# Optimization experiments

Hardware: AMD Instinct MI355X
Metric: run time of the kernel (lower is better)

## Reference

```python
import jax, jax.numpy as jnp
import numpy as np
from jax import lax

B, N, CIN, MID, OUT, G, H, CHILDS = 16, 1024, 256, 512, 256, 4, 1, 512


def _ln(x, g, b, eps=1e-6):
    m = x.mean(-1, keepdims=True)
    v = ((x - m) ** 2).mean(-1, keepdims=True)
    return (x - m) / jnp.sqrt(v + eps) * g + b


def _gconv(x, W, b):
    # grouped 1x1 conv1d: x [B,Cin,N], W [Cout, Cin//G], b [Cout]
    Bb, Cin, Nn = x.shape
    Cout = W.shape[0]
    xg = x.reshape(Bb, G, Cin // G, Nn)
    Wg = W.reshape(G, Cout // G, Cin // G)
    y = jnp.einsum('bgcn,goc->bgon', xg, Wg).reshape(Bb, Cout, Nn)
    return y + b[None, :, None]


def _forward(x, masks_roi1, masks_roi2, score_mask, gt_feat,
             W_att, b_att, W1, b1, W2, b2, g1, beta1, g2, beta2, Wg, bg):
    dt = x.dtype
    # gt branch
    gts = jax.nn.relu(gt_feat @ Wg + bg)  # [B,N,OUT]

    mr1 = masks_roi1 * score_mask[:, None, :]
    mr2 = masks_roi2 * score_mask[:, None, :]

    # attention logits without materializing the [B,N,N,2C] concat:
    # ft[b,i,j] = cat(x[b,j], x[b,i]);  logits = ft @ W_att + b_att
    Wq, Wk = W_att[:CIN], W_att[CIN:]
    lj = jnp.einsum('bjc,ch->bjh', x, Wq)  # query part (varies over j)
    li = jnp.einsum('bic,ch->bih', x, Wk)  # key part   (varies over i)
    attn = jax.nn.sigmoid(lj[:, None, :, :] + li[:, :, None, :] + b_att)  # [B,N,N,H]

    attn1 = attn * mr1[:, :, :, None]
    attn2 = attn * mr2[:, :, :, None]

    # torch fancy-index assign atten_mask[:,:,idces,:]=1 reduces to: any column
    # index appearing in ANY topk index set gets 1 along dim 2 for all b,i,h.
    k4, k2 = CHILDS // 4, CHILDS // 2
    a1 = jnp.moveaxis(attn1, 2, 3)  # [B,N,H,N] -> topk over last axis (= dim 2)
    a2 = jnp.moveaxis(attn2, 2, 3)
    idx1 = lax.top_k(a1, k4)[1]
    idx1m = lax.top_k(-a1, k4)[1]
    idx2 = lax.top_k(a2, k2)[1]
    idx2m = lax.top_k(-a2, k4)[1]
    all_idx = jnp.concatenate([idx1.ravel(), idx1m.ravel(), idx2.ravel(), idx2m.ravel()])
    col = jnp.zeros((N,), dtype=dt).at[all_idx].set(1.0)

    attn = attn * (mr1 + mr2)[:, :, :, None] * col[None, None, :, None]

    f = (score_mask == 0).astype(dt)  # [B,N]
    f_diag = f[:, :, None] * jnp.eye(N, dtype=dt)  # diag_embed
    atten = (attn + f_diag[:, :, :, None]) / CHILDS
    atten = jnp.transpose(atten, (0, 3, 2, 1))  # [B,H,Nj,Ni]

    x_t = jnp.transpose(x, (0, 2, 1))  # [B,CIN,N]
    o1 = jax.nn.relu(_gconv(x_t, W1, b1))  # [B,MID,N]
    o1m = jnp.matmul(o1.reshape(B, H, MID // H, N), atten).reshape(B, MID, N)
    o1m = _ln(jnp.transpose(o1m, (0, 2, 1)), g1, beta1)  # [B,N,MID]
    o1 = o1 + jnp.transpose(o1m, (0, 2, 1))

    o2 = jax.nn.relu(_gconv(o1, W2, b2))  # [B,OUT,N]
    o2m = jnp.matmul(o2.reshape(B, H, OUT // H, N), atten).reshape(B, OUT, N)
    node_feat = _ln(jnp.transpose(o2m, (0, 2, 1)), g2, beta2)  # [B,N,OUT]
    o2 = o2 + jnp.transpose(node_feat, (0, 2, 1))
    output2 = jnp.transpose(o2, (0, 2, 1))  # [B,N,OUT]
    return output2, gts, node_feat


def setup_inputs() -> dict:
    key = jax.random.key(0)
    ks = jax.random.split(key, 16)
    x = jax.random.normal(ks[0], (B, N, CIN), jnp.float32)
    masks_roi1 = (jax.random.uniform(ks[1], (B, N, N)) < 0.1).astype(jnp.float32)
    masks_roi2 = (jax.random.uniform(ks[2], (B, N, N)) < 0.1).astype(jnp.float32)
    score_mask = (jax.random.uniform(ks[3], (B, N)) < 0.8).astype(jnp.float32)
    gt_feat = jax.random.normal(ks[4], (B, N, CIN), jnp.float32)
    s = 0.05
    W_att = jax.random.normal(ks[5], (2 * CIN, H), jnp.float32) * s
    b_att = jnp.zeros((H,), jnp.float32)
    W1 = jax.random.normal(ks[6], (MID, CIN // G), jnp.float32) * s
    b1 = jax.random.normal(ks[7], (MID,), jnp.float32) * s
    W2 = jax.random.normal(ks[8], (OUT, MID // G), jnp.float32) * s
    b2 = jax.random.normal(ks[9], (OUT,), jnp.float32) * s
    g1 = jax.random.normal(ks[10], (MID,), jnp.float32) * s
    beta1 = jnp.zeros((MID,), jnp.float32)
    g2 = jax.random.normal(ks[11], (OUT,), jnp.float32) * s
    beta2 = jnp.zeros((OUT,), jnp.float32)
    Wg = jax.random.normal(ks[12], (CIN, OUT), jnp.float32) * s
    bg = jax.random.normal(ks[13], (OUT,), jnp.float32) * s
    return {"x": x, "masks_roi1": masks_roi1, "masks_roi2": masks_roi2,
            "score_mask": score_mask, "gt_feat": gt_feat,
            "W_att": W_att, "b_att": b_att, "W1": W1, "b1": b1,
            "W2": W2, "b2": b2, "g1": g1, "beta1": beta1,
            "g2": g2, "beta2": beta2, "Wg": Wg, "bg": bg}


def reference(x, masks_roi1, masks_roi2, score_mask, gt_feat,
              W_att, b_att, W1, b1, W2, b2, g1, beta1, g2, beta2, Wg, bg):
    return _forward(x, masks_roi1, masks_roi2, score_mask, gt_feat,
                    W_att, b_att, W1, b1, W2, b2, g1, beta1, g2, beta2, Wg, bg)
```

## Files before the change

kernel.cpp:

```cpp
#include <hip/hip_runtime.h>
#include <cstddef>
#include <cstdint>

#define B_ 16
#define N_ 1024
#define CIN_ 256
#define MID_ 512
#define OUT_ 256

typedef __attribute__((ext_vector_type(8))) short short8v;
typedef __attribute__((ext_vector_type(4))) float f32x4;

__device__ __forceinline__ float sigf(float z){ return 1.f/(1.f+expf(-z)); }
__device__ __forceinline__ ushort f2bf(float f){
  uint32_t u=__float_as_uint(f);
  uint32_t r=(u + 0x7fffu + ((u>>16)&1u))>>16;
  return (ushort)r;
}
__device__ __forceinline__ float bf2f(ushort u){ return __uint_as_float(((uint32_t)u)<<16); }

__device__ __forceinline__ void async16(void* lds, const void* g){
  __builtin_amdgcn_global_load_lds(
      (const __attribute__((address_space(1))) uint32_t*)g,
      (__attribute__((address_space(3))) uint32_t*)lds,
      16, 0, 0);
}

__global__ __launch_bounds__(256) void k_prep(const float* __restrict__ x,
    const float* __restrict__ Watt, float* __restrict__ lj, float* __restrict__ li)
{
  int bn = blockIdx.x*256 + threadIdx.x;
  const float4* xr = (const float4*)(x + (size_t)bn*CIN_);
  const float4* wq = (const float4*)(Watt);
  const float4* wk = (const float4*)(Watt + CIN_);
  float aq=0.f, ak=0.f;
  #pragma unroll 8
  for(int c=0;c<CIN_/4;++c){
    float4 xv=xr[c]; float4 q=wq[c]; float4 w=wk[c];
    aq += xv.x*q.x+xv.y*q.y+xv.z*q.z+xv.w*q.w;
    ak += xv.x*w.x+xv.y*w.y+xv.z*w.z+xv.w*w.w;
  }
  lj[bn]=aq; li[bn]=ak;
}

__global__ __launch_bounds__(256) void k_cast2(const float* __restrict__ x,
    const float* __restrict__ gt, ushort* __restrict__ xb, ushort* __restrict__ gtb)
{
  int i = blockIdx.x*256 + threadIdx.x;
  int which = i>>20; int idx = i & 1048575;
  float4 v = ((const float4*)(which ? gt : x))[idx];
  ((ushort4*)(which ? gtb : xb))[idx] = make_ushort4(f2bf(v.x), f2bf(v.y), f2bf(v.z), f2bf(v.w));
}

__global__ __launch_bounds__(256) void k_wcast(const float* __restrict__ W1,
    const float* __restrict__ W2, const float* __restrict__ Wg,
    ushort* __restrict__ W1b, ushort* __restrict__ W2b, ushort* __restrict__ WgTb)
{
  int bid=blockIdx.x, t=threadIdx.x;
  if(bid<128){ int i=bid*256+t; W1b[i]=f2bf(W1[i]); }
  else if(bid<256){ int i=(bid-128)*256+t; W2b[i]=f2bf(W2[i]); }
  else { int idx=(bid-256)*256+t; int o=idx>>8, c=idx&255; WgTb[idx]=f2bf(Wg[(size_t)c*OUT_+o]); }
}

__global__ __launch_bounds__(256) void k_col(
    const float* __restrict__ m1, const float* __restrict__ m2,
    const float* __restrict__ sc, const float* __restrict__ lj,
    const float* __restrict__ li, const float* __restrict__ batt,
    float* __restrict__ colf, ushort* __restrict__ mrs)
{
  int wid = threadIdx.x>>6, lane = threadIdx.x&63;
  int row = blockIdx.x*4 + wid; int b = row>>10;
  size_t base = (size_t)row*N_ + lane*16;
  const float4* m1p = (const float4*)(m1+base);
  const float4* m2p = (const float4*)(m2+base);
  const float4* scp = (const float4*)(sc + (b<<10) + lane*16);
  float mr1[16], mr2[16];
  int z1=0, z2=0;
  #pragma unroll
  for(int q=0;q<4;++q){
    float4 a=m1p[q], c=m2p[q], s=scp[q];
    mr1[4*q+0]=a.x*s.x; mr1[4*q+1]=a.y*s.y; mr1[4*q+2]=a.z*s.z; mr1[4*q+3]=a.w*s.w;
    mr2[4*q+0]=c.x*s.x; mr2[4*q+1]=c.y*s.y; mr2[4*q+2]=c.z*s.z; mr2[4*q+3]=c.w*s.w;
    #pragma unroll
    for(int k=0;k<4;++k){ z1 += (mr1[4*q+k]==0.f); z2 += (mr2[4*q+k]==0.f); }
  }
  ushort mb[16];
  #pragma unroll
  for(int k=0;k<16;++k) mb[k]=f2bf(mr1[k]+mr2[k]);
  *(short8v*)(mrs+base)   = *(short8v*)&mb[0];
  *(short8v*)(mrs+base+8) = *(short8v*)&mb[8];
  int s1=z1, s2=z2;
  #pragma unroll
  for(int off=1; off<64; off<<=1){
    int t1=__shfl_up(s1,off), t2=__shfl_up(s2,off);
    if(lane>=off){ s1+=t1; s2+=t2; }
  }
  int excl1=s1-z1, excl2=s2-z2;
  int Z1=__shfl(s1,63), Z2=__shfl(s2,63);
  int P1=1024-Z1, P2=1024-Z2;
  bool rare = (P1>128)||(P2>256)||(Z1<128)||(Z2<128);
  if(!rare){
    int zb1=excl1, zb2=excl2;
    #pragma unroll
    for(int k=0;k<16;++k){
      bool q = (mr1[k]!=0.f) || (zb1<128) || (mr2[k]!=0.f) || (zb2<128) || (P2+zb2<256);
      if(q) colf[lane*16+k]=1.0f;
      zb1 += (mr1[k]==0.f); zb2 += (mr2[k]==0.f);
    }
  } else {
    float lir=li[row], ba=batt[0];
    const float* m1r = m1 + (size_t)row*N_;
    const float* m2r = m2 + (size_t)row*N_;
    const float* scr = sc + (b<<10);
    const float* ljr = lj + (b<<10);
    float a1v[16], a2v[16];
    #pragma unroll
    for(int k=0;k<16;++k){
      float v = sigf(ljr[lane*16+k]+lir+ba);
      a1v[k]=mr1[k]*v; a2v[k]=mr2[k]*v;
    }
    for(int k=0;k<16;++k){
      int j = lane*16+k;
      int c1=0,c1m=0,c2=0,c2m=0;
      for(int jp=0;jp<N_;++jp){
        float sv=scr[jp];
        float vv=sigf(ljr[jp]+lir+ba);
        float p1=m1r[jp]*sv*vv, p2=m2r[jp]*sv*vv;
        bool lo = jp<j;
        c1 += (p1>a1v[k])||((p1==a1v[k])&&lo);
        c1m+= (p1<a1v[k])||((p1==a1v[k])&&lo);
        c2 += (p2>a2v[k])||((p2==a2v[k])&&lo);
        c2m+= (p2<a2v[k])||((p2==a2v[k])&&lo);
      }
      if(c1<128||c1m<128||c2<256||c2m<128) colf[j]=1.0f;
    }
  }
}

__global__ __launch_bounds__(256) void k_at(const ushort* __restrict__ mrs,
    const float* __restrict__ sc, const float* __restrict__ lj,
    const float* __restrict__ li, const float* __restrict__ batt,
    const float* __restrict__ colf, ushort* __restrict__ Atb)
{
  int row=blockIdx.x, t=threadIdx.x; int b=row>>10, i=row&1023;
  size_t base=(size_t)row*N_ + 4*t;
  ushort4 mv=*(const ushort4*)(mrs+base);
  float4 ljv=*(const float4*)(lj + (b<<10) + 4*t);
  float4 cv =*(const float4*)(colf + 4*t);
  float lir=li[row], ba=batt[0];
  float fi = (sc[(b<<10)+i]==0.f)?1.f:0.f;
  float mra[4]={bf2f(mv.x),bf2f(mv.y),bf2f(mv.z),bf2f(mv.w)};
  float ljr[4]={ljv.x,ljv.y,ljv.z,ljv.w};
  float cr[4]={cv.x,cv.y,cv.z,cv.w};
  ushort o[4]; int j0=4*t;
  #pragma unroll
  for(int k=0;k<4;++k){
    float v=sigf(ljr[k]+lir+ba);
    float val=v*mra[k]*cr[k];
    if(j0+k==i) val+=fi;
    o[k]=f2bf(val*(1.f/512.f));
  }
  *(ushort4*)(Atb+base) = make_ushort4(o[0],o[1],o[2],o[3]);
}

template<int BM,int BN,int WR,int WC>
__global__ __launch_bounds__(256) void mgemm(
    const ushort* __restrict__ A, int lda, long long sAb, long long sAg,
    const ushort* __restrict__ Bp, int ldb, long long sBb, long long sBg,
    float* __restrict__ C, ushort* __restrict__ Cb, int ldc, long long sCb, long long sCg,
    int K, int nG,
    const float* __restrict__ biasM, int biasMG,
    const float* __restrict__ biasN, int relu)
{
  static_assert(WR*WC==4 && BM==WR*64 && BN==WC*64, "tile");
  __shared__ __align__(16) ushort As[BM*32];
  __shared__ __align__(16) ushort Bs[BN*32];
  int z=blockIdx.z, b=z/nG, g=z%nG;
  A  += (size_t)b*sAb + (size_t)g*sAg;
  Bp += (size_t)b*sBb + (size_t)g*sBg;
  size_t cOff = (size_t)b*sCb + (size_t)g*sCg;
  int m0 = blockIdx.y*BM, n0 = blockIdx.x*BN;
  int tid=threadIdx.x, w=tid>>6, lane=tid&63;
  int la=lane&15, hi=lane>>4;
  int wr=w/WC, wc=w%WC;
  f32x4 acc[4][4] = {};
  constexpr int RND = (BM+BN)/64;
  int srow = lane>>2;
  int sk8  = (lane&3)*8;
  for(int k0=0;k0<K;k0+=32){
    #pragma unroll
    for(int r=0;r<RND;++r){
      int row0 = r*64 + w*16;
      if(row0 < BM){
        const ushort* src = A + (size_t)(m0+row0+srow)*lda + k0 + sk8;
        async16((char*)As + row0*64, src);
      } else {
        const ushort* src = Bp + (size_t)(n0+row0-BM+srow)*ldb + k0 + sk8;
        async16((char*)Bs + (row0-BM)*64, src);
      }
    }
    __syncthreads();
    short8v af[4], bf4[4];
    #pragma unroll
    for(int i2=0;i2<4;++i2) af[i2] = *(const short8v*)&As[(wr*64+i2*16+la)*32 + hi*8];
    #pragma unroll
    for(int j2=0;j2<4;++j2) bf4[j2] = *(const short8v*)&Bs[(wc*64+j2*16+la)*32 + hi*8];
    #pragma unroll
    for(int i2=0;i2<4;++i2)
      #pragma unroll
      for(int j2=0;j2<4;++j2)
        acc[i2][j2] = __builtin_amdgcn_mfma_f32_16x16x32_bf16(af[i2], bf4[j2], acc[i2][j2], 0,0,0);
    __syncthreads();
  }
  #pragma unroll
  for(int i2=0;i2<4;++i2){
    int row0 = m0 + wr*64 + i2*16 + hi*4;
    #pragma unroll
    for(int j2=0;j2<4;++j2){
      int col = n0 + wc*64 + j2*16 + la;
      float bn = biasN ? biasN[col] : 0.f;
      #pragma unroll
      for(int r=0;r<4;++r){
        int row = row0 + r;
        float v = acc[i2][j2][r] + bn + (biasM ? biasM[(size_t)g*biasMG + row] : 0.f);
        if(relu) v = fmaxf(v, 0.f);
        if(C)  C [cOff + (size_t)row*ldc + col] = v;
        if(Cb) Cb[cOff + (size_t)row*ldc + col] = f2bf(v);
      }
    }
  }
}

__global__ __launch_bounds__(256) void k_ln1(const float* __restrict__ o1mT,
    const ushort* __restrict__ o1b,
    const float* __restrict__ g1v, const float* __restrict__ be1, ushort* __restrict__ o1pb)
{
  int row=blockIdx.x, t=threadIdx.x; int b=row>>10, i=row&1023;
  float2 v = ((const float2*)(o1mT + (size_t)row*MID_))[t];
  float s=v.x+v.y, s2=v.x*v.x+v.y*v.y;
  for(int off=32; off; off>>=1){ s+=__shfl_down(s,off); s2+=__shfl_down(s2,off); }
  __shared__ float sm[8];
  int lane=t&63, wid=t>>6;
  if(lane==0){ sm[wid]=s; sm[4+wid]=s2; }
  __syncthreads();
  s=sm[0]+sm[1]+sm[2]+sm[3]; s2=sm[4]+sm[5]+sm[6]+sm[7];
  float mean=s*(1.f/MID_), var=s2*(1.f/MID_)-mean*mean;
  float rstd=rsqrtf(var+1e-6f);
  int m0=2*t;
  float a0=(v.x-mean)*rstd*g1v[m0]+be1[m0];
  float a1=(v.y-mean)*rstd*g1v[m0+1]+be1[m0+1];
  float r0 = bf2f(o1b[((size_t)(b*MID_+m0  ))*N_ + i]);
  float r1 = bf2f(o1b[((size_t)(b*MID_+m0+1))*N_ + i]);
  ushort2 o; o.x=f2bf(a0+r0); o.y=f2bf(a1+r1);
  ((ushort2*)(o1pb + (size_t)row*MID_))[t] = o;
}

__global__ __launch_bounds__(256) void k_ln2f(const float* __restrict__ o2mT,
    const ushort* __restrict__ o2b,
    const float* __restrict__ g2v, const float* __restrict__ be2,
    float* __restrict__ node, float* __restrict__ out2)
{
  int row=blockIdx.x, t=threadIdx.x; int b=row>>10, i=row&1023;
  float v = o2mT[(size_t)row*OUT_ + t];
  float s=v, s2=v*v;
  for(int off=32; off; off>>=1){ s+=__shfl_down(s,off); s2+=__shfl_down(s2,off); }
  __shared__ float sm[8];
  int lane=t&63, wid=t>>6;
  if(lane==0){ sm[wid]=s; sm[4+wid]=s2; }
  __syncthreads();
  s=sm[0]+sm[1]+sm[2]+sm[3]; s2=sm[4]+sm[5]+sm[6]+sm[7];
  float mean=s*(1.f/OUT_); float var=s2*(1.f/OUT_)-mean*mean;
  float rstd=rsqrtf(var+1e-6f);
  float nf=(v-mean)*rstd*g2v[t]+be2[t];
  size_t ro=(size_t)row*OUT_+t;
  node[ro]=nf;
  out2[ro]=nf + bf2f(o2b[((size_t)(b*OUT_+t))*N_ + i]);
}

extern "C" void kernel_launch(void* const* d_in, const int* in_sizes, int n_in,
                              void* d_out, int out_size, void* d_ws, size_t ws_size,
                              hipStream_t stream)
{
  const float* x    = (const float*)d_in[0];
  const float* m1   = (const float*)d_in[1];
  const float* m2   = (const float*)d_in[2];
  const float* sc   = (const float*)d_in[3];
  const float* gt   = (const float*)d_in[4];
  const float* Watt = (const float*)d_in[5];
  const float* batt = (const float*)d_in[6];
  const float* W1   = (const float*)d_in[7];
  const float* b1   = (const float*)d_in[8];
  const float* W2   = (const float*)d_in[9];
  const float* b2   = (const float*)d_in[10];
  const float* g1   = (const float*)d_in[11];
  const float* be1  = (const float*)d_in[12];
  const float* g2   = (const float*)d_in[13];
  const float* be2  = (const float*)d_in[14];
  const float* Wg   = (const float*)d_in[15];
  const float* bg   = (const float*)d_in[16];

  float* out2 = (float*)d_out;
  float* gtso = out2 + (size_t)B_*N_*OUT_;
  float* node = gtso + (size_t)B_*N_*OUT_;

  char* ws = (char*)d_ws;
  float*  colf = (float*)(ws);
  float*  lj   = (float*)(ws + 4096);
  float*  li   = (float*)(ws + 69632);
  ushort* W1b  = (ushort*)(ws + 135168);
  ushort* W2b  = (ushort*)(ws + 200704);
  ushort* WgTb = (ushort*)(ws + 266240);
  char* R1 = ws + 1048576;
  ushort* mrs  = (ushort*)R1;
  float*  o1mT = (float*)R1;
  ushort* Atb  = (ushort*)(ws + 34603008);
  char* R3 = ws + 68157440;
  ushort* xb  = (ushort*)R3;
  ushort* gtb = (ushort*)(R3 + 8388608);
  ushort* o2b = (ushort*)R3;
  ushort* o1b = (ushort*)(ws + 84934656);
  char* R5 = ws + 101711872;
  ushort* o1pb = (ushort*)R5;
  float*  o2mT = (float*)R5;

  hipMemsetAsync(colf, 0, 4096, stream);
  k_prep <<<dim3(B_*N_/256),dim3(256),0,stream>>>(x,Watt,lj,li);
  k_cast2<<<dim3(8192),dim3(256),0,stream>>>(x, gt, xb, gtb);
  k_wcast<<<dim3(512),dim3(256),0,stream>>>(W1, W2, Wg, W1b, W2b, WgTb);
  k_col  <<<dim3(B_*N_/4),dim3(256),0,stream>>>(m1,m2,sc,lj,li,batt,colf,mrs);
  k_at   <<<dim3(B_*N_),dim3(256),0,stream>>>(mrs,sc,lj,li,batt,colf,Atb);

  mgemm<128,128,2,2><<<dim3(2,128,1),256,0,stream>>>(
      gtb, CIN_, 0,0,
      WgTb, CIN_, 0,0,
      gtso, (ushort*)0, OUT_, 0,0,
      CIN_, 1, nullptr,0, bg, 1);

  mgemm<128,128,2,2><<<dim3(8,1,B_*4),256,0,stream>>>(
      W1b, 64, 0, (long long)128*64,
      xb, CIN_, (long long)N_*CIN_, 64,
      (float*)0, o1b, N_, (long long)MID_*N_, (long long)128*N_,
      64, 4, b1, 128, nullptr, 1);

  mgemm<128,128,2,2><<<dim3(4,8,B_),256,0,stream>>>(
      Atb, N_, (long long)N_*N_, 0,
      o1b, N_, (long long)MID_*N_, 0,
      o1mT, (ushort*)0, MID_, (long long)N_*MID_, 0,
      N_, 1, nullptr,0, nullptr, 0);

  k_ln1<<<dim3(B_*N_),256,0,stream>>>(o1mT, o1b, g1, be1, o1pb);

  mgemm<64,256,1,4><<<dim3(4,1,B_*4),256,0,stream>>>(
      W2b, 128, 0, (long long)64*128,
      o1pb, MID_, (long long)N_*MID_, 128,
      (float*)0, o2b, N_, (long long)OUT_*N_, (long long)64*N_,
      128, 4, b2, 64, nullptr, 1);

  mgemm<128,128,2,2><<<dim3(2,8,B_),256,0,stream>>>(
      Atb, N_, (long long)N_*N_, 0,
      o2b, N_, (long long)OUT_*N_, 0,
      o2mT, (ushort*)0, OUT_, (long long)N_*OUT_, 0,
      N_, 1, nullptr,0, nullptr, 0);

  k_ln2f<<<dim3(B_*N_),256,0,stream>>>(o2mT, o2b, g2, be2, node, out2);
}
```

Measured before the change: 465.2 us.

## Fuse prep/cast kernels, widen GEMM K-tile, emit transposed residuals, rework column mask

The separate projection and cast kernels are merged into one kernel that uses a wave per row with a shuffle reduction. The column-mask kernel now assigns one block per row, with a cross-wave prefix scan and a single fused pass over j'. The GEMM takes a K-tile of 64 and a flat async-load mapping, so each stage does more MFMA work per barrier. The o1/o2 GEMMs also write a transposed bf16 copy so the layer-norm kernels can read residuals coalesced instead of with strided gathers. The cost is extra epilogue writes, with uncoalesced transposed stores, plus more LDS per block.

Result: faster. 398.4 us (-14.4%).

```diff
diff --git a/kernel.cpp b/kernel.cpp
--- a/kernel.cpp
+++ b/kernel.cpp
@@ -26,30 +26,30 @@
       16, 0, 0);
 }
 
-__global__ __launch_bounds__(256) void k_prep(const float* __restrict__ x,
-    const float* __restrict__ Watt, float* __restrict__ lj, float* __restrict__ li)
-{
-  int bn = blockIdx.x*256 + threadIdx.x;
-  const float4* xr = (const float4*)(x + (size_t)bn*CIN_);
-  const float4* wq = (const float4*)(Watt);
-  const float4* wk = (const float4*)(Watt + CIN_);
-  float aq=0.f, ak=0.f;
-  #pragma unroll 8
-  for(int c=0;c<CIN_/4;++c){
-    float4 xv=xr[c]; float4 q=wq[c]; float4 w=wk[c];
-    aq += xv.x*q.x+xv.y*q.y+xv.z*q.z+xv.w*q.w;
-    ak += xv.x*w.x+xv.y*w.y+xv.z*w.z+xv.w*w.w;
-  }
-  lj[bn]=aq; li[bn]=ak;
-}
-
-__global__ __launch_bounds__(256) void k_cast2(const float* __restrict__ x,
-    const float* __restrict__ gt, ushort* __restrict__ xb, ushort* __restrict__ gtb)
-{
-  int i = blockIdx.x*256 + threadIdx.x;
-  int which = i>>20; int idx = i & 1048575;
-  float4 v = ((const float4*)(which ? gt : x))[idx];
-  ((ushort4*)(which ? gtb : xb))[idx] = make_ushort4(f2bf(v.x), f2bf(v.y), f2bf(v.z), f2bf(v.w));
+__global__ __launch_bounds__(256) void k_pc(const float* __restrict__ x,
+    const float* __restrict__ gt, const float* __restrict__ Watt,
+    float* __restrict__ lj, float* __restrict__ li,
+    ushort* __restrict__ xb, ushort* __restrict__ gtb)
+{
+  int bid=blockIdx.x, wid=threadIdx.x>>6, lane=threadIdx.x&63;
+  if(bid < 4096){
+    int row = bid*4 + wid;
+    float4 xv = ((const float4*)(x + (size_t)row*CIN_))[lane];
+    ((ushort4*)(xb + (size_t)row*CIN_))[lane] =
+        make_ushort4(f2bf(xv.x), f2bf(xv.y), f2bf(xv.z), f2bf(xv.w));
+    float4 q = ((const float4*)Watt)[lane];
+    float4 w = ((const float4*)(Watt + CIN_))[lane];
+    float aq = xv.x*q.x+xv.y*q.y+xv.z*q.z+xv.w*q.w;
+    float ak = xv.x*w.x+xv.y*w.y+xv.z*w.z+xv.w*w.w;
+    #pragma unroll
+    for(int off=32; off; off>>=1){ aq += __shfl_xor(aq,off); ak += __shfl_xor(ak,off); }
+    if(lane==0){ lj[row]=aq; li[row]=ak; }
+  } else {
+    int row = (bid-4096)*4 + wid;
+    float4 v = ((const float4*)(gt + (size_t)row*CIN_))[lane];
+    ((ushort4*)(gtb + (size_t)row*CIN_))[lane] =
+        make_ushort4(f2bf(v.x), f2bf(v.y), f2bf(v.z), f2bf(v.w));
+  }
 }
 
 __global__ __launch_bounds__(256) void k_wcast(const float* __restrict__ W1,
@@ -68,43 +68,43 @@
     const float* __restrict__ li, const float* __restrict__ batt,
     float* __restrict__ colf, ushort* __restrict__ mrs)
 {
-  int wid = threadIdx.x>>6, lane = threadIdx.x&63;
-  int row = blockIdx.x*4 + wid; int b = row>>10;
-  size_t base = (size_t)row*N_ + lane*16;
-  const float4* m1p = (const float4*)(m1+base);
-  const float4* m2p = (const float4*)(m2+base);
-  const float4* scp = (const float4*)(sc + (b<<10) + lane*16);
-  float mr1[16], mr2[16];
-  int z1=0, z2=0;
-  #pragma unroll
-  for(int q=0;q<4;++q){
-    float4 a=m1p[q], c=m2p[q], s=scp[q];
-    mr1[4*q+0]=a.x*s.x; mr1[4*q+1]=a.y*s.y; mr1[4*q+2]=a.z*s.z; mr1[4*q+3]=a.w*s.w;
-    mr2[4*q+0]=c.x*s.x; mr2[4*q+1]=c.y*s.y; mr2[4*q+2]=c.z*s.z; mr2[4*q+3]=c.w*s.w;
-    #pragma unroll
-    for(int k=0;k<4;++k){ z1 += (mr1[4*q+k]==0.f); z2 += (mr2[4*q+k]==0.f); }
-  }
-  ushort mb[16];
-  #pragma unroll
-  for(int k=0;k<16;++k) mb[k]=f2bf(mr1[k]+mr2[k]);
-  *(short8v*)(mrs+base)   = *(short8v*)&mb[0];
-  *(short8v*)(mrs+base+8) = *(short8v*)&mb[8];
-  int s1=z1, s2=z2;
+  int row = blockIdx.x; int b = row >> 10; int t = threadIdx.x;
+  int lane = t&63, wid = t>>6;
+  size_t base = (size_t)row*N_ + 4*t;
+  float4 m1v = *(const float4*)(m1 + base);
+  float4 m2v = *(const float4*)(m2 + base);
+  float4 scv = *(const float4*)(sc + (b<<10) + 4*t);
+  float mr1[4] = {m1v.x*scv.x, m1v.y*scv.y, m1v.z*scv.z, m1v.w*scv.w};
+  float mr2[4] = {m2v.x*scv.x, m2v.y*scv.y, m2v.z*scv.z, m2v.w*scv.w};
+  *(ushort4*)(mrs + base) = make_ushort4(f2bf(mr1[0]+mr2[0]), f2bf(mr1[1]+mr2[1]),
+                                         f2bf(mr1[2]+mr2[2]), f2bf(mr1[3]+mr2[3]));
+  int z1=0,z2=0;
+  #pragma unroll
+  for(int k=0;k<4;++k){ z1 += (mr1[k]==0.f); z2 += (mr2[k]==0.f); }
+  int s = z1 | (z2<<16);
   #pragma unroll
   for(int off=1; off<64; off<<=1){
-    int t1=__shfl_up(s1,off), t2=__shfl_up(s2,off);
-    if(lane>=off){ s1+=t1; s2+=t2; }
-  }
-  int excl1=s1-z1, excl2=s2-z2;
-  int Z1=__shfl(s1,63), Z2=__shfl(s2,63);
-  int P1=1024-Z1, P2=1024-Z2;
+    int u = __shfl_up(s,off);
+    if(lane>=off) s += u;
+  }
+  __shared__ int wsum[4];
+  if(lane==63) wsum[wid]=s;
+  __syncthreads();
+  int prev=0, tot=0;
+  #pragma unroll
+  for(int w2=0;w2<4;++w2){ int v=wsum[w2]; tot+=v; if(w2<wid) prev+=v; }
+  int incl = s + prev;
+  int z1i = incl & 0xffff, z2i = incl >> 16;
+  int excl1 = z1i - z1, excl2 = z2i - z2;
+  int Z1 = tot & 0xffff, Z2 = tot >> 16;
+  int P1 = 1024-Z1, P2 = 1024-Z2;
   bool rare = (P1>128)||(P2>256)||(Z1<128)||(Z2<128);
   if(!rare){
     int zb1=excl1, zb2=excl2;
     #pragma unroll
-    for(int k=0;k<16;++k){
+    for(int k=0;k<4;++k){
       bool q = (mr1[k]!=0.f) || (zb1<128) || (mr2[k]!=0.f) || (zb2<128) || (P2+zb2<256);
-      if(q) colf[lane*16+k]=1.0f;
+      if(q) colf[4*t+k]=1.0f;
       zb1 += (mr1[k]==0.f); zb2 += (mr2[k]==0.f);
     }
   } else {
@@ -113,27 +113,28 @@
     const float* m2r = m2 + (size_t)row*N_;
     const float* scr = sc + (b<<10);
     const float* ljr = lj + (b<<10);
-    float a1v[16], a2v[16];
-    #pragma unroll
-    for(int k=0;k<16;++k){
-      float v = sigf(ljr[lane*16+k]+lir+ba);
+    float a1v[4], a2v[4];
+    #pragma unroll
+    for(int k=0;k<4;++k){
+      float v = sigf(ljr[4*t+k]+lir+ba);
       a1v[k]=mr1[k]*v; a2v[k]=mr2[k]*v;
     }
-    for(int k=0;k<16;++k){
-      int j = lane*16+k;
-      int c1=0,c1m=0,c2=0,c2m=0;
-      for(int jp=0;jp<N_;++jp){
-        float sv=scr[jp];
-        float vv=sigf(ljr[jp]+lir+ba);
-        float p1=m1r[jp]*sv*vv, p2=m2r[jp]*sv*vv;
-        bool lo = jp<j;
-        c1 += (p1>a1v[k])||((p1==a1v[k])&&lo);
-        c1m+= (p1<a1v[k])||((p1==a1v[k])&&lo);
-        c2 += (p2>a2v[k])||((p2==a2v[k])&&lo);
-        c2m+= (p2<a2v[k])||((p2==a2v[k])&&lo);
+    int c1[4]={0,0,0,0}, c1m[4]={0,0,0,0}, c2[4]={0,0,0,0}, c2m[4]={0,0,0,0};
+    for(int jp=0;jp<N_;++jp){
+      float vv = sigf(ljr[jp]+lir+ba);
+      float p1 = m1r[jp]*scr[jp]*vv, p2 = m2r[jp]*scr[jp]*vv;
+      #pragma unroll
+      for(int k=0;k<4;++k){
+        bool lo = jp < 4*t+k;
+        c1[k] += (p1>a1v[k])||((p1==a1v[k])&&lo);
+        c1m[k]+= (p1<a1v[k])||((p1==a1v[k])&&lo);
+        c2[k] += (p2>a2v[k])||((p2==a2v[k])&&lo);
+        c2m[k]+= (p2<a2v[k])||((p2==a2v[k])&&lo);
       }
-      if(c1<128||c1m<128||c2<256||c2m<128) colf[j]=1.0f;
-    }
+    }
+    #pragma unroll
+    for(int k=0;k<4;++k)
+      if(c1[k]<128||c1m[k]<128||c2[k]<256||c2m[k]<128) colf[4*t+k]=1.0f;
   }
 }
 
@@ -163,53 +164,57 @@
   *(ushort4*)(Atb+base) = make_ushort4(o[0],o[1],o[2],o[3]);
 }
 
-template<int BM,int BN,int WR,int WC>
+template<int BM,int BN,int WR,int WC,int BK>
 __global__ __launch_bounds__(256) void mgemm(
     const ushort* __restrict__ A, int lda, long long sAb, long long sAg,
     const ushort* __restrict__ Bp, int ldb, long long sBb, long long sBg,
     float* __restrict__ C, ushort* __restrict__ Cb, int ldc, long long sCb, long long sCg,
+    ushort* __restrict__ CbT, long long sTb, long long sTg, int ldt,
     int K, int nG,
     const float* __restrict__ biasM, int biasMG,
     const float* __restrict__ biasN, int relu)
 {
   static_assert(WR*WC==4 && BM==WR*64 && BN==WC*64, "tile");
-  __shared__ __align__(16) ushort As[BM*32];
-  __shared__ __align__(16) ushort Bs[BN*32];
+  static_assert((BM*BK)%512==0 && (BN*BK)%512==0, "stage align");
+  __shared__ __align__(16) ushort As[BM*BK];
+  __shared__ __align__(16) ushort Bs[BN*BK];
   int z=blockIdx.z, b=z/nG, g=z%nG;
   A  += (size_t)b*sAb + (size_t)g*sAg;
   Bp += (size_t)b*sBb + (size_t)g*sBg;
   size_t cOff = (size_t)b*sCb + (size_t)g*sCg;
+  size_t tOff = (size_t)b*sTb + (size_t)g*sTg;
   int m0 = blockIdx.y*BM, n0 = blockIdx.x*BN;
   int tid=threadIdx.x, w=tid>>6, lane=tid&63;
   int la=lane&15, hi=lane>>4;
   int wr=w/WC, wc=w%WC;
   f32x4 acc[4][4] = {};
-  constexpr int RND = (BM+BN)/64;
-  int srow = lane>>2;
-  int sk8  = (lane&3)*8;
-  for(int k0=0;k0<K;k0+=32){
-    #pragma unroll
-    for(int r=0;r<RND;++r){
-      int row0 = r*64 + w*16;
-      if(row0 < BM){
-        const ushort* src = A + (size_t)(m0+row0+srow)*lda + k0 + sk8;
-        async16((char*)As + row0*64, src);
+  constexpr int ISS = (BM+BN)*BK/2048;
+  for(int k0=0;k0<K;k0+=BK){
+    #pragma unroll
+    for(int r=0;r<ISS;++r){
+      int e = (r*256 + tid)*8;
+      if(e < BM*BK){
+        int row=e/BK, kk=e%BK;
+        async16((char*)As + (size_t)e*2, A + (size_t)(m0+row)*lda + k0+kk);
       } else {
-        const ushort* src = Bp + (size_t)(n0+row0-BM+srow)*ldb + k0 + sk8;
-        async16((char*)Bs + (row0-BM)*64, src);
+        int e2=e-BM*BK; int row=e2/BK, kk=e2%BK;
+        async16((char*)Bs + (size_t)e2*2, Bp + (size_t)(n0+row)*ldb + k0+kk);
       }
     }
     __syncthreads();
-    short8v af[4], bf4[4];
-    #pragma unroll
-    for(int i2=0;i2<4;++i2) af[i2] = *(const short8v*)&As[(wr*64+i2*16+la)*32 + hi*8];
-    #pragma unroll
-    for(int j2=0;j2<4;++j2) bf4[j2] = *(const short8v*)&Bs[(wc*64+j2*16+la)*32 + hi*8];
-    #pragma unroll
-    for(int i2=0;i2<4;++i2)
-      #pragma unroll
-      for(int j2=0;j2<4;++j2)
-        acc[i2][j2] = __builtin_amdgcn_mfma_f32_16x16x32_bf16(af[i2], bf4[j2], acc[i2][j2], 0,0,0);
+    #pragma unroll
+    for(int h=0;h<BK/32;++h){
+      short8v af[4], bf4[4];
+      #pragma unroll
+      for(int i2=0;i2<4;++i2) af[i2] = *(const short8v*)&As[(wr*64+i2*16+la)*BK + h*32 + hi*8];
+      #pragma unroll
+      for(int j2=0;j2<4;++j2) bf4[j2] = *(const short8v*)&Bs[(wc*64+j2*16+la)*BK + h*32 + hi*8];
+      #pragma unroll
+      for(int i2=0;i2<4;++i2)
+        #pragma unroll
+        for(int j2=0;j2<4;++j2)
+          acc[i2][j2] = __builtin_amdgcn_mfma_f32_16x16x32_bf16(af[i2], bf4[j2], acc[i2][j2], 0,0,0);
+    }
     __syncthreads();
   }
   #pragma unroll
@@ -224,18 +229,19 @@
         int row = row0 + r;
         float v = acc[i2][j2][r] + bn + (biasM ? biasM[(size_t)g*biasMG + row] : 0.f);
         if(relu) v = fmaxf(v, 0.f);
-        if(C)  C [cOff + (size_t)row*ldc + col] = v;
-        if(Cb) Cb[cOff + (size_t)row*ldc + col] = f2bf(v);
+        if(C)   C  [cOff + (size_t)row*ldc + col] = v;
+        if(Cb)  Cb [cOff + (size_t)row*ldc + col] = f2bf(v);
+        if(CbT) CbT[tOff + (size_t)col*ldt + row] = f2bf(v);
       }
     }
   }
 }
 
 __global__ __launch_bounds__(256) void k_ln1(const float* __restrict__ o1mT,
-    const ushort* __restrict__ o1b,
+    const ushort* __restrict__ o1bT,
     const float* __restrict__ g1v, const float* __restrict__ be1, ushort* __restrict__ o1pb)
 {
-  int row=blockIdx.x, t=threadIdx.x; int b=row>>10, i=row&1023;
+  int row=blockIdx.x, t=threadIdx.x;
   float2 v = ((const float2*)(o1mT + (size_t)row*MID_))[t];
   float s=v.x+v.y, s2=v.x*v.x+v.y*v.y;
   for(int off=32; off; off>>=1){ s+=__shfl_down(s,off); s2+=__shfl_down(s2,off); }
@@ -249,18 +255,17 @@
   int m0=2*t;
   float a0=(v.x-mean)*rstd*g1v[m0]+be1[m0];
   float a1=(v.y-mean)*rstd*g1v[m0+1]+be1[m0+1];
-  float r0 = bf2f(o1b[((size_t)(b*MID_+m0  ))*N_ + i]);
-  float r1 = bf2f(o1b[((size_t)(b*MID_+m0+1))*N_ + i]);
-  ushort2 o; o.x=f2bf(a0+r0); o.y=f2bf(a1+r1);
+  ushort2 rr = ((const ushort2*)(o1bT + (size_t)row*MID_))[t];
+  ushort2 o; o.x=f2bf(a0+bf2f(rr.x)); o.y=f2bf(a1+bf2f(rr.y));
   ((ushort2*)(o1pb + (size_t)row*MID_))[t] = o;
 }
 
 __global__ __launch_bounds__(256) void k_ln2f(const float* __restrict__ o2mT,
-    const ushort* __restrict__ o2b,
+    const ushort* __restrict__ o2bT,
     const float* __restrict__ g2v, const float* __restrict__ be2,
     float* __restrict__ node, float* __restrict__ out2)
 {
-  int row=blockIdx.x, t=threadIdx.x; int b=row>>10, i=row&1023;
+  int row=blockIdx.x, t=threadIdx.x;
   float v = o2mT[(size_t)row*OUT_ + t];
   float s=v, s2=v*v;
   for(int off=32; off; off>>=1){ s+=__shfl_down(s,off); s2+=__shfl_down(s2,off); }
@@ -274,7 +279,7 @@
   float nf=(v-mean)*rstd*g2v[t]+be2[t];
   size_t ro=(size_t)row*OUT_+t;
   node[ro]=nf;
-  out2[ro]=nf + bf2f(o2b[((size_t)(b*OUT_+t))*N_ + i]);
+  out2[ro]=nf + bf2f(o2bT[ro]);
 }
 
 extern "C" void kernel_launch(void* const* d_in, const int* in_sizes, int n_in,
@@ -315,52 +320,59 @@
   float*  o1mT = (float*)R1;
   ushort* Atb  = (ushort*)(ws + 34603008);
   char* R3 = ws + 68157440;
-  ushort* xb  = (ushort*)R3;
-  ushort* gtb = (ushort*)(R3 + 8388608);
-  ushort* o2b = (ushort*)R3;
-  ushort* o1b = (ushort*)(ws + 84934656);
+  ushort* xb   = (ushort*)R3;
+  ushort* gtb  = (ushort*)(R3 + 8388608);
+  ushort* o2b  = (ushort*)R3;
+  ushort* o2bT = (ushort*)(R3 + 8388608);
+  char* R4 = ws + 84934656;
+  ushort* o1b  = (ushort*)R4;
+  ushort* o1pb = (ushort*)R4;
   char* R5 = ws + 101711872;
-  ushort* o1pb = (ushort*)R5;
+  ushort* o1bT = (ushort*)R5;
   float*  o2mT = (float*)R5;
 
   hipMemsetAsync(colf, 0, 4096, stream);
-  k_prep <<<dim3(B_*N_/256),dim3(256),0,stream>>>(x,Watt,lj,li);
-  k_cast2<<<dim3(8192),dim3(256),0,stream>>>(x, gt, xb, gtb);
+  k_pc   <<<dim3(8192),dim3(256),0,stream>>>(x, gt, Watt, lj, li, xb, gtb);
   k_wcast<<<dim3(512),dim3(256),0,stream>>>(W1, W2, Wg, W1b, W2b, WgTb);
-  k_col  <<<dim3(B_*N_/4),dim3(256),0,stream>>>(m1,m2,sc,lj,li,batt,colf,mrs);
+  k_col  <<<dim3(B_*N_),dim3(256),0,stream>>>(m1,m2,sc,lj,li,batt,colf,mrs);
   k_at   <<<dim3(B_*N_),dim3(256),0,stream>>>(mrs,sc,lj,li,batt,colf,Atb);
 
-  mgemm<128,128,2,2><<<dim3(2,128,1),256,0,stream>>>(
+  mgemm<128,128,2,2,64><<<dim3(2,128,1),256,0,stream>>>(
       gtb, CIN_, 0,0,
       WgTb, CIN_, 0,0,
       gtso, (ushort*)0, OUT_, 0,0,
+      (ushort*)0, 0,0,0,
       CIN_, 1, nullptr,0, bg, 1);
 
-  mgemm<128,128,2,2><<<dim3(8,1,B_*4),256,0,stream>>>(
+  mgemm<128,128,2,2,64><<<dim3(8,1,B_*4),256,0,stream>>>(
       W1b, 64, 0, (long long)128*64,
       xb, CIN_, (long long)N_*CIN_, 64,
       (float*)0, o1b, N_, (long long)MID_*N_, (long long)128*N_,
+      o1bT, (long long)N_*MID_, 128, MID_,
       64, 4, b1, 128, nullptr, 1);
 
-  mgemm<128,128,2,2><<<dim3(4,8,B_),256,0,stream>>>(
+  mgemm<128,128,2,2,64><<<dim3(4,8,B_),256,0,stream>>>(
       Atb, N_, (long long)N_*N_, 0,
       o1b, N_, (long long)MID_*N_, 0,
       o1mT, (ushort*)0, MID_, (long long)N_*MID_, 0,
+      (ushort*)0, 0,0,0,
       N_, 1, nullptr,0, nullptr, 0);
 
-  k_ln1<<<dim3(B_*N_),256,0,stream>>>(o1mT, o1b, g1, be1, o1pb);
-
-  mgemm<64,256,1,4><<<dim3(4,1,B_*4),256,0,stream>>>(
+  k_ln1<<<dim3(B_*N_),256,0,stream>>>(o1mT, o1bT, g1, be1, o1pb);
+
+  mgemm<64,256,1,4,64><<<dim3(4,1,B_*4),256,0,stream>>>(
       W2b, 128, 0, (long long)64*128,
       o1pb, MID_, (long long)N_*MID_, 128,
       (float*)0, o2b, N_, (long long)OUT_*N_, (long long)64*N_,
+      o2bT, (long long)N_*OUT_, 64, OUT_,
       128, 4, b2, 64, nullptr, 1);
 
-  mgemm<128,128,2,2><<<dim3(2,8,B_),256,0,stream>>>(
+  mgemm<128,128,2,2,64><<<dim3(2,8,B_),256,0,stream>>>(
       Atb, N_, (long long)N_*N_, 0,
       o2b, N_, (long long)OUT_*N_, 0,
       o2mT, (ushort*)0, OUT_, (long long)N_*OUT_, 0,
+      (ushort*)0, 0,0,0,
       N_, 1, nullptr,0, nullptr, 0);
 
-  k_ln2f<<<dim3(B_*N_),256,0,stream>>>(o2mT, o2b, g2, be2, node, out2);
-}
+  k_ln2f<<<dim3(B_*N_),256,0,stream>>>(o2mT, o2bT, g2, be2, node, out2);
+}
```
